# Optimization experiments

Hardware: AMD Instinct MI355X
Metric: run time of the kernel (lower is better)

## Reference

```python
import jax
import jax.numpy as jnp
import numpy as np
from jax import lax

EPS = 0.1
MAX_ITER = 50
LOG_EPS = 1e-8


def _l2_normalize(a):
    # matches torch.nn.functional.normalize(p=2, dim=1) with eps=1e-12
    n = jnp.linalg.norm(a, axis=1, keepdims=True)
    return a / jnp.maximum(n, 1e-12)


def setup_inputs() -> dict:
    key = jax.random.key(0)
    k1, k2, k3 = jax.random.split(key, 3)
    B, K, D = 65536, 256, 128
    return {
        "x": jax.random.normal(k1, (B, D), dtype=jnp.float32),
        "prototypes": jax.random.normal(k2, (K, D), dtype=jnp.float32),
        "coordinates": jax.random.normal(k3, (B, K), dtype=jnp.float32),
    }


def reference(x, prototypes, coordinates):
    B = x.shape[0]
    K = prototypes.shape[0]
    # cosine cost matrix C: (B, K)
    xn = _l2_normalize(x)
    yn = _l2_normalize(prototypes)
    C = 1.0 - xn @ yn.T
    K_mat = jnp.exp(-C / EPS)
    logK = jnp.log(K_mat + LOG_EPS)  # (B, K)
    log_mu = jnp.log(1.0 / B + LOG_EPS)  # scalar (uniform marginals)
    log_nu = jnp.log(1.0 / K + LOG_EPS)

    def step(carry, _):
        u, v = carry
        u = log_mu - jax.scipy.special.logsumexp(logK + v[None, :], axis=1)
        v = log_nu - jax.scipy.special.logsumexp(logK + u[:, None], axis=0)
        return (u, v), None

    (u, v), _ = lax.scan(
        step,
        (jnp.zeros((B,), dtype=x.dtype), jnp.zeros((K,), dtype=x.dtype)),
        None,
        length=MAX_ITER,
    )
    pi = jnp.exp(u[:, None] + logK + v[None, :])  # (B, K) transport plan
    coord_weights = jax.nn.softmax(jnp.abs(coordinates), axis=1)
    return (pi * C * coord_weights).sum()
```

## Files before the change

### kernel.cpp

```cpp
#include <hip/hip_runtime.h>
#include <hip/hip_fp16.h>

#define B_N 65536
#define K_N 256
#define D_N 128
#define N_ITER 50
#define NSHARD 16
#define NBLK 256
#define BUFSTRIDE (NSHARD * K_N)
#define EVPAD 20

#define BAR_U (64 * 16)

constexpr float MU_EPS = 1.0f / 65536.0f + 1e-8f;
constexpr float NU_EPS = 1.0f / 256.0f + 1e-8f;
constexpr float KSCALE = 8192.0f;
constexpr float INV_KSCALE = 1.0f / 8192.0f;
constexpr float NUKS = NU_EPS * KSCALE;
constexpr float MUKS = MU_EPS * KSCALE;

typedef __attribute__((ext_vector_type(8))) short bf16x8;
typedef __attribute__((ext_vector_type(4))) float f32x4;
typedef __attribute__((ext_vector_type(4))) unsigned u32x4;

union frag_u { uint4 u; bf16x8 v; };

__device__ __forceinline__ float wave_sum(float v) {
#pragma unroll
    for (int m = 1; m < 64; m <<= 1) v += __shfl_xor(v, m, 64);
    return v;
}

__device__ __forceinline__ short f32_to_bf16(float x) {
    unsigned u = __float_as_uint(x);
    return (short)((u + 0x7FFFu + ((u >> 16) & 1u)) >> 16);
}
__device__ __forceinline__ float bf16_hi_f32(float x) {
    unsigned u = __float_as_uint(x);
    unsigned r = ((u + 0x7FFFu + ((u >> 16) & 1u)) >> 16) << 16;
    return __uint_as_float(r);
}

__global__ __launch_bounds__(64) void proto_norm_init(
        const float* __restrict__ proto, short* __restrict__ bh_s,
        short* __restrict__ bl_s, float* __restrict__ csbuf,
        unsigned* __restrict__ bar, float* __restrict__ out) {
    const int blk = blockIdx.x;
    const int lane = threadIdx.x;
    if (blk < 256) {
        float2 p = *(const float2*)&proto[blk * 128 + lane * 2];
        float ss = wave_sum(p.x * p.x + p.y * p.y);
        float inv = 1.0f / fmaxf(sqrtf(ss), 1e-12f);
        float v0 = p.x * inv, v1 = p.y * inv;
        short2 h, l;
        h.x = f32_to_bf16(v0); h.y = f32_to_bf16(v1);
        l.x = f32_to_bf16(v0 - bf16_hi_f32(v0));
        l.y = f32_to_bf16(v1 - bf16_hi_f32(v1));
        const int k0 = lane * 2;
        const int ks = k0 >> 5, qq = (k0 >> 3) & 3, j = k0 & 7;
        const int mm = blk & 15, CT = blk >> 4;
        const size_t off = (size_t)(((CT * 4 + ks) * 64 + qq * 16 + mm)) * 8 + j;
        *(short2*)&bh_s[off] = h;
        *(short2*)&bl_s[off] = l;
    } else {
        for (int i = lane; i < BAR_U; i += 64) bar[i] = 0u;
        for (int i = lane; i < 3 * BUFSTRIDE; i += 64)
            csbuf[i] = (i >= 2 * BUFSTRIDE && i < 2 * BUFSTRIDE + K_N) ? NUKS : 0.0f;
        if (lane == 0) out[0] = 0.0f;
    }
}

__global__ __launch_bounds__(1024, 4) void sinkhorn_persist(
        const float* __restrict__ x, const short* __restrict__ bh_s,
        const short* __restrict__ bl_s, float* __restrict__ csbuf,
        const float* __restrict__ coord, unsigned* __restrict__ bar,
        float* __restrict__ out) {
    __shared__ __align__(16) float ev_lds[16 * EVPAD];
    __shared__ float cs_lds[16 * 273];
    __shared__ float wpart[16];
    const int blk = blockIdx.x, tid = threadIdx.x;
    const int w = tid >> 6, lane = tid & 63;
    const int q = lane >> 4, m = lane & 15;

    const int arow = blk * 256 + w * 16 + m;
    float av[4][8];
    float ss = 0.0f;
#pragma unroll
    for (int ks = 0; ks < 4; ks++) {
        const float* ap = &x[(size_t)arow * 128 + ks * 32 + q * 8];
        float4 a0 = *(const float4*)ap;
        float4 a1 = *(const float4*)(ap + 4);
        av[ks][0] = a0.x; av[ks][1] = a0.y; av[ks][2] = a0.z; av[ks][3] = a0.w;
        av[ks][4] = a1.x; av[ks][5] = a1.y; av[ks][6] = a1.z; av[ks][7] = a1.w;
#pragma unroll
        for (int j = 0; j < 8; j++) ss = fmaf(av[ks][j], av[ks][j], ss);
    }
    ss += __shfl_xor(ss, 16, 64);
    ss += __shfl_xor(ss, 32, 64);
    const float rnv = 1.0f / fmaxf(sqrtf(ss), 1e-12f);
    frag_u ah[4], al[4];
#pragma unroll
    for (int ks = 0; ks < 4; ks++) {
        unsigned uh[4], ul[4];
#pragma unroll
        for (int p = 0; p < 4; p++) {
            float a0 = av[ks][2 * p] * rnv;
            float a1 = av[ks][2 * p + 1] * rnv;
            unsigned u;
            asm("v_cvt_pk_bf16_f32 %0, %1, %2" : "=v"(u) : "v"(a0), "v"(a1));
            float h0 = __uint_as_float(u << 16);
            float h1 = __uint_as_float(u & 0xffff0000u);
            float l0 = a0 - h0, l1 = a1 - h1;
            unsigned u2;
            asm("v_cvt_pk_bf16_f32 %0, %1, %2" : "=v"(u2) : "v"(l0), "v"(l1));
            uh[p] = u; ul[p] = u2;
        }
        ah[ks].u = make_uint4(uh[0], uh[1], uh[2], uh[3]);
        al[ks].u = make_uint4(ul[0], ul[1], ul[2], ul[3]);
    }
    float kvf[4][16];
    {
        f32x4 acc[16];
#pragma unroll
        for (int CT = 0; CT < 16; CT++) acc[CT] = (f32x4){0.f, 0.f, 0.f, 0.f};
#pragma unroll
        for (int ks = 0; ks < 4; ks++) {
#pragma unroll
            for (int CT = 0; CT < 16; CT++) {
                const size_t off = (size_t)(((CT * 4 + ks) * 64 + lane)) * 8;
                bf16x8 bh = *(const bf16x8*)&bh_s[off];
                bf16x8 bl = *(const bf16x8*)&bl_s[off];
                acc[CT] = __builtin_amdgcn_mfma_f32_16x16x32_bf16(ah[ks].v, bh, acc[CT], 0, 0, 0);
                acc[CT] = __builtin_amdgcn_mfma_f32_16x16x32_bf16(al[ks].v, bh, acc[CT], 0, 0, 0);
                acc[CT] = __builtin_amdgcn_mfma_f32_16x16x32_bf16(ah[ks].v, bl, acc[CT], 0, 0, 0);
            }
        }
#pragma unroll
        for (int CT = 0; CT < 16; CT++) {
#pragma unroll
            for (int r = 0; r < 4; r++) {
                float Cv = 1.0f - acc[CT][r];
                kvf[r][CT] = KSCALE * (__expf(-10.0f * Cv) + 1e-8f);
            }
        }
    }

    float ai_reg[4] = {0.f, 0.f, 0.f, 0.f};
    bool dead = false;
    for (int t = 0; t < N_ITER; t++) {
        const int p_read = (t + 2) % 3, p_acc = t % 3, p_zero = (t + 1) % 3;
        if (tid < 256) {
            const float* cb = csbuf + p_read * BUFSTRIDE;
            float cs = 0.0f;
#pragma unroll
            for (int s = 0; s < NSHARD; s++)
                cs += __hip_atomic_load(&cb[s * 256 + tid], __ATOMIC_RELAXED,
                                        __HIP_MEMORY_SCOPE_AGENT);
            ev_lds[(tid >> 4) * EVPAD + (tid & 15)] = NUKS * __builtin_amdgcn_rcpf(cs);
        }
        if (blk < NSHARD && tid < 256)
            __hip_atomic_store(&csbuf[p_zero * BUFSTRIDE + blk * 256 + tid], 0.0f,
                               __ATOMIC_RELAXED, __HIP_MEMORY_SCOPE_AGENT);
        __syncthreads();
        float e[16];
#pragma unroll
        for (int j = 0; j < 16; j++) e[j] = ev_lds[j * EVPAD + m];
        float acc[16];
#pragma unroll
        for (int j = 0; j < 16; j++) acc[j] = 0.0f;
#pragma unroll
        for (int rg = 0; rg < 4; rg++) {
            float part = 0.0f;
#pragma unroll
            for (int j = 0; j < 16; j++) part = fmaf(kvf[rg][j], e[j], part);
            part += __shfl_xor(part, 8, 64);
            part += __shfl_xor(part, 4, 64);
            part += __shfl_xor(part, 2, 64);
            part += __shfl_xor(part, 1, 64);
            float ai = MUKS * __builtin_amdgcn_rcpf(part);
            ai_reg[rg] = ai;
#pragma unroll
            for (int j = 0; j < 16; j++) acc[j] = fmaf(kvf[rg][j], ai, acc[j]);
        }
#pragma unroll
        for (int j = 0; j < 16; j++) {
            acc[j] += __shfl_xor(acc[j], 16, 64);
            acc[j] += __shfl_xor(acc[j], 32, 64);
        }
        if (q == 0) {
#pragma unroll
            for (int j = 0; j < 16; j++) cs_lds[w * 273 + j * 17 + m] = acc[j];
        }
        __syncthreads();
        if (tid < 256) {
            float v = 0.0f;
#pragma unroll
            for (int p = 0; p < 16; p++) v += cs_lds[p * 273 + (tid >> 4) * 17 + (tid & 15)];
            atomicAdd(&csbuf[p_acc * BUFSTRIDE + (blk & (NSHARD - 1)) * 256 + tid], v);
        }
        __syncthreads();
        if (tid == 0)
            __hip_atomic_store(&bar[(blk & 63) * 16 + (blk >> 6)], (unsigned)(t + 1),
                               __ATOMIC_RELAXED, __HIP_MEMORY_SCOPE_AGENT);
        if (w == 0 && !dead) {
            const unsigned T = (unsigned)(t + 1);
            const unsigned* ap = &bar[lane * 16];
            long long t0 = __builtin_amdgcn_s_memrealtime();
            while (true) {
                u32x4 v;
                asm volatile("global_load_dwordx4 %0, %1, off sc0 sc1\n\t"
                             "s_waitcnt vmcnt(0)"
                             : "=v"(v) : "v"(ap) : "memory");
                if (__all(v.x >= T && v.y >= T && v.z >= T && v.w >= T)) break;
                __builtin_amdgcn_s_sleep(2);
                if (__builtin_amdgcn_s_memrealtime() - t0 > (1LL << 22)) {
                    dead = true;
                    break;
                }
            }
        }
        __syncthreads();
    }

    if (tid < 256) {
        const float* cb = csbuf + ((N_ITER - 1) % 3) * BUFSTRIDE;
        float cs = 0.0f;
#pragma unroll
        for (int s = 0; s < NSHARD; s++)
            cs += __hip_atomic_load(&cb[s * 256 + tid], __ATOMIC_RELAXED,
                                    __HIP_MEMORY_SCOPE_AGENT);
        ev_lds[(tid >> 4) * EVPAD + (tid & 15)] = NUKS * __builtin_amdgcn_rcpf(cs);
    }
    __syncthreads();
    float ef[16];
#pragma unroll
    for (int j = 0; j < 16; j++) ef[j] = ev_lds[j * EVPAD + m];
    float accv = 0.0f;
#pragma unroll
    for (int rg = 0; rg < 4; rg++) {
        const int row = blk * 256 + w * 16 + q * 4 + rg;
        float a[16];
#pragma unroll
        for (int j = 0; j < 16; j++)
            a[j] = fabsf(coord[(size_t)row * 256 + j * 16 + m]);
        float mx = a[0];
#pragma unroll
        for (int j = 1; j < 16; j++) mx = fmaxf(mx, a[j]);
        mx = fmaxf(mx, __shfl_xor(mx, 8, 64));
        mx = fmaxf(mx, __shfl_xor(mx, 4, 64));
        mx = fmaxf(mx, __shfl_xor(mx, 2, 64));
        mx = fmaxf(mx, __shfl_xor(mx, 1, 64));
        float ex[16];
        float zs = 0.0f;
#pragma unroll
        for (int j = 0; j < 16; j++) { ex[j] = __expf(a[j] - mx); zs += ex[j]; }
        zs += __shfl_xor(zs, 8, 64);
        zs += __shfl_xor(zs, 4, 64);
        zs += __shfl_xor(zs, 2, 64);
        zs += __shfl_xor(zs, 1, 64);
        float s = 0.0f;
#pragma unroll
        for (int j = 0; j < 16; j++) {
            float Cj = -0.1f * __logf(kvf[rg][j] * INV_KSCALE - 1e-8f);
            s += kvf[rg][j] * ef[j] * Cj * ex[j];
        }
        accv = fmaf(s, ai_reg[rg] * INV_KSCALE * __builtin_amdgcn_rcpf(zs), accv);
    }
    accv = wave_sum(accv);
    if (lane == 0) wpart[w] = accv;
    __syncthreads();
    if (tid == 0) {
        float tot = 0.0f;
#pragma unroll
        for (int i = 0; i < 16; i++) tot += wpart[i];
        atomicAdd(out, tot);
    }
}

extern "C" void kernel_launch(void* const* d_in, const int* in_sizes, int n_in,
                              void* d_out, int out_size, void* d_ws, size_t ws_size,
                              hipStream_t stream) {
    const float* x = (const float*)d_in[0];
    const float* proto = (const float*)d_in[1];
    const float* coord = (const float*)d_in[2];
    float* out = (float*)d_out;
    char* ws = (char*)d_ws;
    short* bh_s = (short*)(ws + 33554432);
    short* bl_s = bh_s + 32768;
    unsigned* bar = (unsigned*)(ws + 33554432 + 131072 + 262144);
    float* csbuf = (float*)(ws + 33554432 + 131072 + 262144 + 262144);

    hipLaunchKernelGGL(proto_norm_init, dim3(257), dim3(64), 0, stream,
                       proto, bh_s, bl_s, csbuf, bar, out);
    hipLaunchKernelGGL(sinkhorn_persist, dim3(NBLK), dim3(1024), 0, stream,
                       x, bh_s, bl_s, csbuf, coord, bar, out);
}
```

Before: 411.8 us.

## Use DPP row reductions and transposed LDS layouts in Sinkhorn iteration

Replaces the 16-lane shuffle reduction of row partial sums with DPP row operations. Stores the e vector transposed so each lane reads its 16 values as four float4 LDS loads. Drops the cross-quad shuffle reduction of the column accumulators: each quad writes its partials into a larger transposed LDS buffer (256 x 68) and the 256 reducer threads sum 64 slots with float4 reads. The aim is to cut shuffle/ds_bpermute traffic per iteration, at the cost of much more LDS use (about 68 KB), which may limit occupancy or create bank conflicts on the strided writes.

```diff
diff --git a/kernel.cpp b/kernel.cpp
--- a/kernel.cpp
+++ b/kernel.cpp
@@ -9,6 +9,7 @@
 #define NBLK 256
 #define BUFSTRIDE (NSHARD * K_N)
 #define EVPAD 20
+#define CS2_STRIDE 68
 
 #define BAR_U (64 * 16)
 
@@ -28,6 +29,19 @@
 __device__ __forceinline__ float wave_sum(float v) {
 #pragma unroll
     for (int m = 1; m < 64; m <<= 1) v += __shfl_xor(v, m, 64);
+    return v;
+}
+
+__device__ __forceinline__ float dpp_sum16(float v) {
+    int x;
+    x = __builtin_amdgcn_update_dpp(0, __float_as_int(v), 0xB1, 0xF, 0xF, true);
+    v += __int_as_float(x);
+    x = __builtin_amdgcn_update_dpp(0, __float_as_int(v), 0x4E, 0xF, 0xF, true);
+    v += __int_as_float(x);
+    x = __builtin_amdgcn_update_dpp(0, __float_as_int(v), 0x141, 0xF, 0xF, true);
+    v += __int_as_float(x);
+    x = __builtin_amdgcn_update_dpp(0, __float_as_int(v), 0x140, 0xF, 0xF, true);
+    v += __int_as_float(x);
     return v;
 }
 
@@ -76,7 +90,7 @@
         const float* __restrict__ coord, unsigned* __restrict__ bar,
         float* __restrict__ out) {
     __shared__ __align__(16) float ev_lds[16 * EVPAD];
-    __shared__ float cs_lds[16 * 273];
+    __shared__ __align__(16) float cs_lds[256 * CS2_STRIDE];
     __shared__ float wpart[16];
     const int blk = blockIdx.x, tid = threadIdx.x;
     const int w = tid >> 6, lane = tid & 63;
@@ -156,15 +170,21 @@
             for (int s = 0; s < NSHARD; s++)
                 cs += __hip_atomic_load(&cb[s * 256 + tid], __ATOMIC_RELAXED,
                                         __HIP_MEMORY_SCOPE_AGENT);
-            ev_lds[(tid >> 4) * EVPAD + (tid & 15)] = NUKS * __builtin_amdgcn_rcpf(cs);
+            ev_lds[(tid & 15) * EVPAD + (tid >> 4)] = NUKS * __builtin_amdgcn_rcpf(cs);
         }
         if (blk < NSHARD && tid < 256)
             __hip_atomic_store(&csbuf[p_zero * BUFSTRIDE + blk * 256 + tid], 0.0f,
                                __ATOMIC_RELAXED, __HIP_MEMORY_SCOPE_AGENT);
         __syncthreads();
         float e[16];
-#pragma unroll
-        for (int j = 0; j < 16; j++) e[j] = ev_lds[j * EVPAD + m];
+        {
+            const float4* ep = (const float4*)(ev_lds + m * EVPAD);
+            float4 E0 = ep[0], E1 = ep[1], E2 = ep[2], E3 = ep[3];
+            e[0] = E0.x; e[1] = E0.y; e[2] = E0.z; e[3] = E0.w;
+            e[4] = E1.x; e[5] = E1.y; e[6] = E1.z; e[7] = E1.w;
+            e[8] = E2.x; e[9] = E2.y; e[10] = E2.z; e[11] = E2.w;
+            e[12] = E3.x; e[13] = E3.y; e[14] = E3.z; e[15] = E3.w;
+        }
         float acc[16];
 #pragma unroll
         for (int j = 0; j < 16; j++) acc[j] = 0.0f;
@@ -173,29 +193,25 @@
             float part = 0.0f;
 #pragma unroll
             for (int j = 0; j < 16; j++) part = fmaf(kvf[rg][j], e[j], part);
-            part += __shfl_xor(part, 8, 64);
-            part += __shfl_xor(part, 4, 64);
-            part += __shfl_xor(part, 2, 64);
-            part += __shfl_xor(part, 1, 64);
+            part = dpp_sum16(part);
             float ai = MUKS * __builtin_amdgcn_rcpf(part);
             ai_reg[rg] = ai;
 #pragma unroll
             for (int j = 0; j < 16; j++) acc[j] = fmaf(kvf[rg][j], ai, acc[j]);
         }
-#pragma unroll
-        for (int j = 0; j < 16; j++) {
-            acc[j] += __shfl_xor(acc[j], 16, 64);
-            acc[j] += __shfl_xor(acc[j], 32, 64);
-        }
-        if (q == 0) {
-#pragma unroll
-            for (int j = 0; j < 16; j++) cs_lds[w * 273 + j * 17 + m] = acc[j];
-        }
+        const int slot = w * 4 + q;
+#pragma unroll
+        for (int j = 0; j < 16; j++)
+            cs_lds[(j * 16 + m) * CS2_STRIDE + slot] = acc[j];
         __syncthreads();
         if (tid < 256) {
+            const float4* rp = (const float4*)(cs_lds + tid * CS2_STRIDE);
             float v = 0.0f;
 #pragma unroll
-            for (int p = 0; p < 16; p++) v += cs_lds[p * 273 + (tid >> 4) * 17 + (tid & 15)];
+            for (int s4 = 0; s4 < 16; s4++) {
+                float4 s = rp[s4];
+                v += s.x + s.y + s.z + s.w;
+            }
             atomicAdd(&csbuf[p_acc * BUFSTRIDE + (blk & (NSHARD - 1)) * 256 + tid], v);
         }
         __syncthreads();
@@ -229,12 +245,18 @@
         for (int s = 0; s < NSHARD; s++)
             cs += __hip_atomic_load(&cb[s * 256 + tid], __ATOMIC_RELAXED,
                                     __HIP_MEMORY_SCOPE_AGENT);
-        ev_lds[(tid >> 4) * EVPAD + (tid & 15)] = NUKS * __builtin_amdgcn_rcpf(cs);
+        ev_lds[(tid & 15) * EVPAD + (tid >> 4)] = NUKS * __builtin_amdgcn_rcpf(cs);
     }
     __syncthreads();
     float ef[16];
-#pragma unroll
-    for (int j = 0; j < 16; j++) ef[j] = ev_lds[j * EVPAD + m];
+    {
+        const float4* ep = (const float4*)(ev_lds + m * EVPAD);
+        float4 E0 = ep[0], E1 = ep[1], E2 = ep[2], E3 = ep[3];
+        ef[0] = E0.x; ef[1] = E0.y; ef[2] = E0.z; ef[3] = E0.w;
+        ef[4] = E1.x; ef[5] = E1.y; ef[6] = E1.z; ef[7] = E1.w;
+        ef[8] = E2.x; ef[9] = E2.y; ef[10] = E2.z; ef[11] = E2.w;
+        ef[12] = E3.x; ef[13] = E3.y; ef[14] = E3.z; ef[15] = E3.w;
+    }
     float accv = 0.0f;
 #pragma unroll
     for (int rg = 0; rg < 4; rg++) {
```

Result: faster. 350.3 us (-14.9%).
